# Kernel tuning notes

Measured on AMD Instinct MI355X. Metric: run time of the kernel, lower is better.

## Reference

```python
import jax, jax.numpy as jnp
import numpy as np

B, T, D = 2048, 200, 64
H1, H2 = 80, 40
CONST_MIN = -4294967295.0


def setup_inputs() -> dict:
    key = jax.random.key(0)
    ks = jax.random.split(key, 10)
    q = jax.random.normal(ks[0], (B, D), dtype=jnp.float32)
    k = jax.random.normal(ks[1], (B, T, D), dtype=jnp.float32)
    v = jax.random.normal(ks[2], (B, T, D), dtype=jnp.float32)
    mask = jax.random.randint(ks[3], (B, T), 0, 2, dtype=jnp.int32)
    # MLP params: Dense(80, sigmoid) -> Dense(40, sigmoid) -> Dense(1)
    s1 = 1.0 / np.sqrt(4 * D)
    W1 = jax.random.normal(ks[4], (4 * D, H1), dtype=jnp.float32) * s1
    b1 = jnp.zeros((H1,), dtype=jnp.float32)
    W2 = jax.random.normal(ks[5], (H1, H2), dtype=jnp.float32) * (1.0 / np.sqrt(H1))
    b2 = jnp.zeros((H2,), dtype=jnp.float32)
    Wf = jax.random.normal(ks[6], (H2, 1), dtype=jnp.float32) * (1.0 / np.sqrt(H2))
    bf = jnp.zeros((1,), dtype=jnp.float32)
    return {"q": q, "k": k, "v": v, "mask": mask,
            "W1": W1, "b1": b1, "W2": W2, "b2": b2, "Wf": Wf, "bf": bf}


def reference(q, k, v, mask, W1, b1, W2, b2, Wf, bf):
    # q: [B,D] tiled over T -> [B,T,D]
    qt = jnp.broadcast_to(q[:, None, :], k.shape)
    # per-pair features [B,T,4D]
    info = jnp.concatenate([qt, k, qt - k, qt * k], axis=-1)
    h = jax.nn.sigmoid(jnp.einsum('btf,fh->bth', info, W1) + b1)
    h = jax.nn.sigmoid(jnp.einsum('bth,hg->btg', h, W2) + b2)
    logits = (jnp.einsum('btg,go->bto', h, Wf) + bf)[..., 0]  # [B,T]
    logits = jnp.where(mask == 0, jnp.float32(CONST_MIN), logits)
    w = jax.nn.softmax(logits, axis=-1)  # [B,T]
    out = jnp.einsum('bt,btd->bd', w, v)  # weighted sum of v
    return out
```

## Files before the change

### kernel.cpp

```cpp
#include <hip/hip_runtime.h>
#include <math.h>

#define T_LEN 200

typedef short bf8 __attribute__((ext_vector_type(8)));
typedef float f32x4 __attribute__((ext_vector_type(4)));

__device__ __forceinline__ float sigmoidf_(float x){ return 1.0f/(1.0f+__expf(-x)); }
__device__ __forceinline__ unsigned int pk_bf16(float lo, float hi){
  unsigned int r; asm("v_cvt_pk_bf16_f32 %0, %1, %2":"=v"(r):"v"(lo),"v"(hi)); return r;
}
union U4B8 { uint4 u; bf8 b; };
__device__ __forceinline__ bf8 pack8(float4 x, float4 y){
  U4B8 r;
  r.u.x = pk_bf16(x.x,x.y); r.u.y = pk_bf16(x.z,x.w);
  r.u.z = pk_bf16(y.x,y.y); r.u.w = pk_bf16(y.z,y.w);
  return r.b;
}
__device__ __forceinline__ bf8 pack8m(float4 x, float4 qx, float4 y, float4 qy){
  U4B8 r;
  r.u.x = pk_bf16(x.x*qx.x, x.y*qx.y); r.u.y = pk_bf16(x.z*qx.z, x.w*qx.w);
  r.u.z = pk_bf16(y.x*qy.x, y.y*qy.y); r.u.w = pk_bf16(y.z*qy.z, y.w*qy.w);
  return r.b;
}

__global__ void prep_kernel(const float* __restrict__ W1, const float* __restrict__ W2,
                            const float* __restrict__ b2, const float* __restrict__ Wf,
                            float* __restrict__ wsf){
  unsigned short* fb = (unsigned short*)wsf;
  int i = blockIdx.x*256 + threadIdx.x;
  if (i < 15360){
    int fi = i >> 9;
    int lane = (i>>3)&63, e = i&7;
    int ht = fi/6, ks = fi%6;
    int h = ht*16 + (lane&15);
    int f = ks*32 + ((lane>>4)<<3) + e;
    float val;
    if (f < 64)        val = W1[(64+f)*80+h] - W1[(128+f)*80+h];
    else if (f < 128)  val = W1[(128+f)*80+h];
    else               val = W1[(f-128)*80+h] + W1[f*80+h];
    fb[i] = (unsigned short)(pk_bf16(val,val) & 0xffffu);
  }
  if (i < 4608){
    int fi = i >> 9;
    int lane = (i>>3)&63, e = i&7;
    int gt = fi/3, ks = fi%3;
    int g = gt*16 + (lane&15);
    int h = ks*32 + ((lane>>4)<<3) + e;
    float val = (g<40 && h<80) ? W2[h*40+g] : 0.f;
    fb[15360+i] = (unsigned short)(pk_bf16(val,val) & 0xffffu);
  }
  if (i < 48){
    wsf[9984  + i] = (i<40) ? b2[i] : 0.f;
    wsf[10032 + i] = (i<40) ? Wf[i] : 0.f;
  }
}

__global__ __launch_bounds__(64, 1) void fused_kernel(
    const float* __restrict__ q, const float* __restrict__ k, const float* __restrict__ v,
    const int* __restrict__ mask, const float* __restrict__ b1,
    const float* __restrict__ bf, const float* __restrict__ wsf,
    float* __restrict__ out)
{
  __shared__ unsigned short tl[224];
  __shared__ __align__(16) unsigned int Hw[2][16*52];
  __shared__ float e_lds[16];
  __shared__ __align__(16) unsigned int w2s[9*64*4];

  const int lane = threadIdx.x;
  const int lg = lane>>4, lc = lane&15;
  const long b = blockIdx.x;

  const float* kb = k + b*(T_LEN*64);
  const float* vb = v + b*(T_LEN*64);
  const int*   mb = mask + b*T_LEN;
  const float* qb = q + b*64;
  const unsigned short* fbg = (const unsigned short*)wsf;
  const bf8* A1f = (const bf8*)fbg;
  const uint4* A2u = (const uint4*)(fbg + 15360);
  const float* b2p = wsf + 9984;
  const float* wfp = wsf + 10032;

  { uint4 z = {0,0,0,0}; *(uint4*)(&Hw[lane>>5][((lane&31)>>1)*52 + 40 + (lane&1)*4]) = z; }

  #pragma unroll
  for (int i=0;i<9;++i) ((uint4*)w2s)[i*64+lane] = A2u[i*64+lane];

  bf8 wk[20];
  #pragma unroll
  for (int ht=0; ht<5; ++ht)
    #pragma unroll
    for (int j=0; j<4; ++j) wk[ht*4+j] = A1f[(ht*6+j)*64+lane];
  float b2v[12], wfv[12];
  #pragma unroll
  for (int gt=0; gt<3; ++gt){
    float4 bv = *(const float4*)(b2p + gt*16 + lg*4);
    float4 wv = *(const float4*)(wfp + gt*16 + lg*4);
    b2v[gt*4+0]=bv.x; b2v[gt*4+1]=bv.y; b2v[gt*4+2]=bv.z; b2v[gt*4+3]=bv.w;
    wfv[gt*4+0]=wv.x; wfv[gt*4+1]=wv.y; wfv[gt*4+2]=wv.z; wfv[gt*4+3]=wv.w;
  }

  f32x4 qacc[5];
  float4 qA0 = *(const float4*)(qb + lg*8);
  float4 qA1 = *(const float4*)(qb + lg*8 + 4);
  float4 qB0 = *(const float4*)(qb + 32 + lg*8);
  float4 qB1 = *(const float4*)(qb + 32 + lg*8 + 4);
  {
    bf8 fq0 = pack8(qA0,qA1);
    bf8 fq1 = pack8(qB0,qB1);
    #pragma unroll
    for (int ht=0; ht<5; ++ht){
      float4 bv = *(const float4*)(b1 + ht*16 + lg*4);
      qacc[ht][0]=bv.x; qacc[ht][1]=bv.y; qacc[ht][2]=bv.z; qacc[ht][3]=bv.w;
      qacc[ht] = __builtin_amdgcn_mfma_f32_16x16x32_bf16(A1f[(ht*6+4)*64+lane], fq0, qacc[ht],0,0,0);
      qacc[ht] = __builtin_amdgcn_mfma_f32_16x16x32_bf16(A1f[(ht*6+5)*64+lane], fq1, qacc[ht],0,0,0);
    }
  }
  const float bf0 = bf[0];

  int tot = 0;
  unsigned long long ltm = (1ull<<lane) - 1ull;
  #pragma unroll
  for (int c=0;c<4;++c){
    int t = c*64 + lane;
    bool f = (t < T_LEN) && (mb[t] != 0);
    unsigned long long bal = __ballot(f);
    if (f) tl[tot + (int)__popcll(bal & ltm)] = (unsigned short)t;
    tot += (int)__popcll(bal);
  }
  asm volatile("s_waitcnt lgkmcnt(0)" ::: "memory");
  __builtin_amdgcn_sched_barrier(0);

  if (tot == 0){
    float accv = 0.f;
    for (int t=0; t<T_LEN; ++t) accv += vb[t*64 + lane];
    out[b*64 + lane] = accv * (1.0f/(float)T_LEN);
    return;
  }

  int tp = tl[min(lc, tot-1)];
  const float* kr = kb + tp*64 + lg*8;
  float4 na0 = *(const float4*)(kr);
  float4 na1 = *(const float4*)(kr+4);
  float4 nb0 = *(const float4*)(kr+32);
  float4 nb1 = *(const float4*)(kr+36);
  float vcur[16];
  #pragma unroll
  for (int i=0;i<16;++i){
    int ti = tl[min(i, tot-1)];
    vcur[i] = vb[ti*64 + lane];
  }

  float acc_pv0 = 0.f, acc_pv1 = 0.f;
  float se0 = 0.f, se1 = 0.f;
  int buf = 0;
  for (int base = 0; base < tot; base += 16, buf ^= 1){
    const bool have_next = (base + 16 < tot);
    bf8 f0 = pack8(na0,na1);
    bf8 f1 = pack8(nb0,nb1);
    bf8 f2 = pack8m(na0,qA0,na1,qA1);
    bf8 f3 = pack8m(nb0,qB0,nb1,qB1);
    float vnxt[16];
    if (have_next){
      int tn = tl[min(base+16+lc, tot-1)];
      const float* krn = kb + tn*64 + lg*8;
      na0 = *(const float4*)(krn);
      na1 = *(const float4*)(krn+4);
      nb0 = *(const float4*)(krn+32);
      nb1 = *(const float4*)(krn+36);
      #pragma unroll
      for (int i=0;i<16;++i){
        int ti = tl[min(base+16+i, tot-1)];
        vnxt[i] = vb[ti*64 + lane];
      }
    }

    f32x4 acc[5];
    #pragma unroll
    for (int ht=0; ht<5; ++ht) acc[ht] = qacc[ht];
    #pragma unroll
    for (int ht=0; ht<5; ++ht){
      acc[ht] = __builtin_amdgcn_mfma_f32_16x16x32_bf16(wk[ht*4+0], f0, acc[ht],0,0,0);
      acc[ht] = __builtin_amdgcn_mfma_f32_16x16x32_bf16(wk[ht*4+1], f1, acc[ht],0,0,0);
      acc[ht] = __builtin_amdgcn_mfma_f32_16x16x32_bf16(wk[ht*4+2], f2, acc[ht],0,0,0);
      acc[ht] = __builtin_amdgcn_mfma_f32_16x16x32_bf16(wk[ht*4+3], f3, acc[ht],0,0,0);
    }

    unsigned int* Hb = &Hw[buf][0];
    #pragma unroll
    for (int ht=0; ht<5; ++ht){
      #pragma unroll
      for (int rp=0; rp<2; ++rp)
        Hb[lc*52 + ht*8+lg*2+rp] = pk_bf16(sigmoidf_(acc[ht][2*rp]), sigmoidf_(acc[ht][2*rp+1]));
    }
    asm volatile("s_waitcnt lgkmcnt(0)" ::: "memory");
    __builtin_amdgcn_sched_barrier(0);

    bf8 c0[3];
    #pragma unroll
    for (int ks=0; ks<3; ++ks) c0[ks] = *(const bf8*)(Hb + lc*52 + 16*ks + 4*lg);
    f32x4 g0[3];
    #pragma unroll
    for (int gt=0; gt<3; ++gt){
      g0[gt][0]=b2v[gt*4+0]; g0[gt][1]=b2v[gt*4+1]; g0[gt][2]=b2v[gt*4+2]; g0[gt][3]=b2v[gt*4+3];
    }
    #pragma unroll
    for (int gt=0; gt<3; ++gt){
      #pragma unroll
      for (int ks=0; ks<3; ++ks){
        bf8 wf2 = *(const bf8*)(w2s + ((gt*3+ks)*64+lane)*4);
        g0[gt] = __builtin_amdgcn_mfma_f32_16x16x32_bf16(wf2, c0[ks], g0[gt],0,0,0);
      }
    }
    float p0=0.f;
    #pragma unroll
    for (int gt=0; gt<3; ++gt){
      #pragma unroll
      for (int r=0;r<4;++r) p0 = fmaf(wfv[gt*4+r], sigmoidf_(g0[gt][r]), p0);
    }
    p0 += __shfl_xor(p0,16); p0 += __shfl_xor(p0,32);
    if (lg == 0) e_lds[lc] = (base+lc < tot) ? __expf(p0 + bf0) : 0.f;
    asm volatile("s_waitcnt lgkmcnt(0)" ::: "memory");
    __builtin_amdgcn_sched_barrier(0);

    #pragma unroll
    for (int i=0;i<16;i+=2){
      float ei0 = e_lds[i];
      float ei1 = e_lds[i+1];
      se0 += ei0; se1 += ei1;
      acc_pv0 = fmaf(ei0, vcur[i],   acc_pv0);
      acc_pv1 = fmaf(ei1, vcur[i+1], acc_pv1);
    }
    if (have_next){
      #pragma unroll
      for (int i=0;i<16;++i) vcur[i] = vnxt[i];
    }
  }

  out[b*64 + lane] = (acc_pv0 + acc_pv1) / (se0 + se1);
}

extern "C" void kernel_launch(void* const* d_in, const int* in_sizes, int n_in,
                              void* d_out, int out_size, void* d_ws, size_t ws_size,
                              hipStream_t stream) {
  const float* q    = (const float*)d_in[0];
  const float* k    = (const float*)d_in[1];
  const float* v    = (const float*)d_in[2];
  const int*   mask = (const int*)d_in[3];
  const float* W1   = (const float*)d_in[4];
  const float* b1   = (const float*)d_in[5];
  const float* W2   = (const float*)d_in[6];
  const float* b2   = (const float*)d_in[7];
  const float* Wf   = (const float*)d_in[8];
  const float* bf   = (const float*)d_in[9];
  float* out = (float*)d_out;
  float* wsf = (float*)d_ws;

  hipLaunchKernelGGL(prep_kernel, dim3(60), dim3(256), 0, stream, W1, W2, b2, Wf, wsf);
  hipLaunchKernelGGL(fused_kernel, dim3(2048), dim3(64), 0, stream,
                     q, k, v, mask, b1, bf, wsf, out);
}
```

Measured before the change: 39.47 us.

## Split each batch row's sequence across two blocks and combine partials

The fused kernel now launches two single-wave blocks per batch row, each handling half of the 200 timesteps. Each block writes an unnormalized weighted-v partial and an exp-sum partial to workspace, and a new combine kernel adds them and normalizes. The softmax skips max subtraction, so adding partial exp sums directly stays consistent with the original. This doubles the number of waves to improve occupancy and latency hiding on a GPU with many CUs. In exchange it adds a third kernel launch, workspace traffic, and repeats the per-block q projection and weight loads.

Measured after the change: 44.12 us. +11.8%, slower.

```diff
diff --git a/kernel.cpp b/kernel.cpp
--- a/kernel.cpp
+++ b/kernel.cpp
@@ -2,6 +2,8 @@
 #include <math.h>
 
 #define T_LEN 200
+#define SEG 100
+#define NB 2048
 
 typedef short bf8 __attribute__((ext_vector_type(8)));
 typedef float f32x4 __attribute__((ext_vector_type(4)));
@@ -56,20 +58,22 @@
   }
 }
 
-__global__ __launch_bounds__(64, 1) void fused_kernel(
+__global__ __launch_bounds__(64, 1) void fused_partial(
     const float* __restrict__ q, const float* __restrict__ k, const float* __restrict__ v,
     const int* __restrict__ mask, const float* __restrict__ b1,
     const float* __restrict__ bf, const float* __restrict__ wsf,
-    float* __restrict__ out)
+    float* __restrict__ pvp, float* __restrict__ sep)
 {
-  __shared__ unsigned short tl[224];
+  __shared__ unsigned short tl[112];
   __shared__ __align__(16) unsigned int Hw[2][16*52];
   __shared__ float e_lds[16];
   __shared__ __align__(16) unsigned int w2s[9*64*4];
 
   const int lane = threadIdx.x;
   const int lg = lane>>4, lc = lane&15;
-  const long b = blockIdx.x;
+  const int bid = blockIdx.x;
+  const long b = bid >> 1;
+  const int tbase = (bid & 1) * SEG;
 
   const float* kb = k + b*(T_LEN*64);
   const float* vb = v + b*(T_LEN*64);
@@ -118,23 +122,21 @@
   }
   const float bf0 = bf[0];
 
-  int tot = 0;
   unsigned long long ltm = (1ull<<lane) - 1ull;
-  #pragma unroll
-  for (int c=0;c<4;++c){
-    int t = c*64 + lane;
-    bool f = (t < T_LEN) && (mb[t] != 0);
-    unsigned long long bal = __ballot(f);
-    if (f) tl[tot + (int)__popcll(bal & ltm)] = (unsigned short)t;
-    tot += (int)__popcll(bal);
-  }
+  bool f0m = (mb[tbase + lane] != 0);
+  unsigned long long bal0 = __ballot(f0m);
+  bool f1m = (lane < SEG-64) && (mb[tbase + 64 + lane] != 0);
+  unsigned long long bal1 = __ballot(f1m);
+  int c0n = (int)__popcll(bal0);
+  int tot = c0n + (int)__popcll(bal1);
+  if (f0m) tl[(int)__popcll(bal0 & ltm)] = (unsigned short)(tbase + lane);
+  if (f1m) tl[c0n + (int)__popcll(bal1 & ltm)] = (unsigned short)(tbase + 64 + lane);
   asm volatile("s_waitcnt lgkmcnt(0)" ::: "memory");
   __builtin_amdgcn_sched_barrier(0);
 
   if (tot == 0){
-    float accv = 0.f;
-    for (int t=0; t<T_LEN; ++t) accv += vb[t*64 + lane];
-    out[b*64 + lane] = accv * (1.0f/(float)T_LEN);
+    pvp[(long)bid*64 + lane] = 0.f;
+    if (lane == 0) sep[bid] = 0.f;
     return;
   }
 
@@ -237,7 +239,26 @@
     }
   }
 
-  out[b*64 + lane] = (acc_pv0 + acc_pv1) / (se0 + se1);
+  pvp[(long)bid*64 + lane] = acc_pv0 + acc_pv1;
+  if (lane == 0) sep[bid] = se0 + se1;
+}
+
+__global__ __launch_bounds__(64) void combine_kernel(
+    const float* __restrict__ v, const float* __restrict__ pvp,
+    const float* __restrict__ sep, float* __restrict__ out)
+{
+  const int lane = threadIdx.x;
+  const long b = blockIdx.x;
+  float se = sep[2*b] + sep[2*b+1];
+  float pv = pvp[(2*b)*64 + lane] + pvp[(2*b+1)*64 + lane];
+  if (se > 0.f){
+    out[b*64 + lane] = pv / se;
+  } else {
+    const float* vb = v + b*(T_LEN*64);
+    float accv = 0.f;
+    for (int t=0; t<T_LEN; ++t) accv += vb[t*64 + lane];
+    out[b*64 + lane] = accv * (1.0f/(float)T_LEN);
+  }
 }
 
 extern "C" void kernel_launch(void* const* d_in, const int* in_sizes, int n_in,
@@ -255,8 +276,12 @@
   const float* bf   = (const float*)d_in[9];
   float* out = (float*)d_out;
   float* wsf = (float*)d_ws;
+  float* pvp = wsf + 10240;
+  float* sep = wsf + 10240 + 4096*64;
 
   hipLaunchKernelGGL(prep_kernel, dim3(60), dim3(256), 0, stream, W1, W2, b2, Wf, wsf);
-  hipLaunchKernelGGL(fused_kernel, dim3(2048), dim3(64), 0, stream,
-                     q, k, v, mask, b1, bf, wsf, out);
-}
+  hipLaunchKernelGGL(fused_partial, dim3(NB*2), dim3(64), 0, stream,
+                     q, k, v, mask, b1, bf, wsf, pvp, sep);
+  hipLaunchKernelGGL(combine_kernel, dim3(NB), dim3(64), 0, stream,
+                     v, pvp, sep, out);
+}
```
